# Performance work log

Measured on AMD Instinct MI355X. Metric: run time of the kernel, lower is better.

Reference implementation:

```python
import jax, jax.numpy as jnp
import numpy as np

N, H, C, E, R = 16384, 1024, 256, 16, 128
EPS = 1e-8


def setup_inputs() -> dict:
    key = jax.random.key(0)
    ks = jax.random.split(key, 8)
    s = 1.0 / np.sqrt(H)
    return {
        "x": jax.random.normal(ks[0], (N, H), jnp.float32),
        "Wd": jax.random.normal(ks[1], (H, C), jnp.float32) * s,
        "bd": jax.random.normal(ks[2], (C,), jnp.float32) * 0.01,
        "centroids": jax.random.uniform(ks[3], (E, C), jnp.float32),  # torch.rand
        "Wg": jax.random.normal(ks[4], (E, H, H), jnp.float32) * s,
        "bg": jax.random.normal(ks[5], (E, H), jnp.float32) * 0.01,
        "U": jax.random.normal(ks[6], (E, H, R), jnp.float32) * s,
        "V": jax.random.normal(ks[7], (E, R, H), jnp.float32) * (1.0 / np.sqrt(R)),
        "k": 2,
    }


def reference(x, Wd, bd, centroids, Wg, bg, U, V, k):
    # ---- Router ----
    distilled = jax.nn.gelu(x @ Wd + bd, approximate=False)          # [N, C]
    dn = distilled / jnp.maximum(
        jnp.linalg.norm(distilled, axis=-1, keepdims=True), EPS)
    cn = centroids / jnp.maximum(
        jnp.linalg.norm(centroids, axis=-1, keepdims=True), EPS)
    # cdist (euclidean) between dn [N,C] and cn [E,C]
    d2 = (jnp.sum(dn * dn, -1, keepdims=True)
          + jnp.sum(cn * cn, -1)[None, :]
          - 2.0 * (dn @ cn.T))                                        # [N, E]
    distances = jnp.sqrt(jnp.maximum(d2, 0.0))
    probabilities = jax.nn.softmax(-distances, axis=-1)               # [N, E]
    top_p, top_i = jax.lax.top_k(probabilities, k)                    # [N, k]
    # sparse combine weights: zero except at top-k experts
    combine = jnp.zeros((x.shape[0], E), x.dtype)
    combine = combine.at[jnp.arange(x.shape[0])[:, None], top_i].set(top_p)
    # ---- Expert dispatch: scan over experts (low-rank Highway blocks) ----
    def body(acc, params):
        Wg_e, bg_e, U_e, V_e, w_e = params
        gate = jax.nn.sigmoid(x @ Wg_e + bg_e)                        # [N, H]
        trans = (x @ U_e) @ V_e                                       # [N, H]
        y = gate * trans + (1.0 - gate) * x
        return acc + w_e[:, None] * y, None
    out, _ = jax.lax.scan(body, jnp.zeros_like(x),
                          (Wg, bg, U, V, combine.T))
    return out
```

## Files before the change

kernel.cpp:

```cpp
#include <hip/hip_runtime.h>
#include <hip/hip_bf16.h>
#include <hip/hip_fp16.h>
#include <cstdint>
#include <cstddef>

#define NTOK 16384
#define HD   1024
#define CD   256
#define NE   16
#define RD   128
#define MAXBLK 528
#define EGRID  2304

typedef __attribute__((ext_vector_type(8))) short bf16x8;
typedef __attribute__((ext_vector_type(4))) float f32x4;
typedef unsigned short u16;
typedef unsigned int u32;

__device__ __forceinline__ u16 f2bf(float f) {
    u32 u = __float_as_uint(f);
    u32 r = (u + 0x7FFFu + ((u >> 16) & 1u)) >> 16;
    return (u16)r;
}

__device__ __forceinline__ void gload16(const void* g, void* lds) {
    __builtin_amdgcn_global_load_lds((const __attribute__((address_space(1))) void*)g,
                                     (__attribute__((address_space(3))) void*)lds,
                                     16, 0, 0);
}

__device__ __forceinline__ float wredsum(float v) {
#pragma unroll
    for (int m = 32; m >= 1; m >>= 1) v += __shfl_xor(v, m, 64);
    return v;
}

__global__ __launch_bounds__(64) void centroid_norm_kernel(
    const float* __restrict__ cen, float* __restrict__ cn, float* __restrict__ sncn)
{
    int e = blockIdx.x, l = threadIdx.x;
    float4 c = *(const float4*)&cen[e * CD + l * 4];
    float ss = wredsum(c.x * c.x + c.y * c.y + c.z * c.z + c.w * c.w);
    float den = fmaxf(sqrtf(ss), 1e-8f);
    float4 n;
    n.x = c.x / den; n.y = c.y / den; n.z = c.z / den; n.w = c.w / den;
    *(float4*)&cn[e * CD + l * 4] = n;
    float s2 = wredsum(n.x * n.x + n.y * n.y + n.z * n.z + n.w * n.w);
    if (l == 0) sncn[e] = s2;
}

__global__ __launch_bounds__(256, 4) void router_gemm_kernel(
    const float* __restrict__ x, const float* __restrict__ Wd,
    const float* __restrict__ bd, float* __restrict__ dT)
{
    __shared__ float lA[16][128];
    __shared__ float lB[16][64];
    int tid = threadIdx.x;
    int rb = (blockIdx.x >> 2) * 128;
    int cb = (blockIdx.x & 3) * 64;
    int tx = tid & 15, ty = tid >> 4;
    int arow = tid >> 1, akq = (tid & 1) * 8;
    int bk = tid >> 4, bc = (tid & 15) * 4;
    float acc[8][4];
#pragma unroll
    for (int i = 0; i < 8; ++i)
#pragma unroll
        for (int j = 0; j < 4; ++j) acc[i][j] = 0.f;

    for (int k0 = 0; k0 < HD; k0 += 16) {
        float4 a0 = *(const float4*)&x[(size_t)(rb + arow) * HD + k0 + akq];
        float4 a1 = *(const float4*)&x[(size_t)(rb + arow) * HD + k0 + akq + 4];
        float4 bv = *(const float4*)&Wd[(size_t)(k0 + bk) * CD + cb + bc];
        __syncthreads();
        lA[akq + 0][arow] = a0.x; lA[akq + 1][arow] = a0.y;
        lA[akq + 2][arow] = a0.z; lA[akq + 3][arow] = a0.w;
        lA[akq + 4][arow] = a1.x; lA[akq + 5][arow] = a1.y;
        lA[akq + 6][arow] = a1.z; lA[akq + 7][arow] = a1.w;
        *(float4*)&lB[bk][bc] = bv;
        __syncthreads();
#pragma unroll
        for (int kk = 0; kk < 16; ++kk) {
            float4 va0 = *(const float4*)&lA[kk][ty * 8];
            float4 va1 = *(const float4*)&lA[kk][ty * 8 + 4];
            float4 vb  = *(const float4*)&lB[kk][tx * 4];
            float ar[8] = {va0.x, va0.y, va0.z, va0.w, va1.x, va1.y, va1.z, va1.w};
            float br[4] = {vb.x, vb.y, vb.z, vb.w};
#pragma unroll
            for (int i = 0; i < 8; ++i)
#pragma unroll
                for (int j = 0; j < 4; ++j) acc[i][j] = fmaf(ar[i], br[j], acc[i][j]);
        }
    }
#pragma unroll
    for (int j = 0; j < 4; ++j) {
        int c = cb + tx * 4 + j;
        float b = bd[c];
        float g[8];
#pragma unroll
        for (int i = 0; i < 8; ++i) {
            float v = acc[i][j] + b;
            g[i] = 0.5f * v * (1.f + erff(v * 0.70710678118654752f));
        }
        float4 w0 = {g[0], g[1], g[2], g[3]};
        float4 w1 = {g[4], g[5], g[6], g[7]};
        *(float4*)&dT[(size_t)c * NTOK + rb + ty * 8] = w0;
        *(float4*)&dT[(size_t)c * NTOK + rb + ty * 8 + 4] = w1;
    }
}

__global__ __launch_bounds__(256) void router_score_kernel(
    const float* __restrict__ dT, const float* __restrict__ cn,
    const float* __restrict__ sncn, int* __restrict__ top_i,
    float* __restrict__ top_w, int* __restrict__ counts)
{
    __shared__ float lcn[NE][CD];
    __shared__ float sdot[NE][64];
    __shared__ float sss[64];
    __shared__ int hist[NE];
    int tid = threadIdx.x, lane = tid & 63, w = tid >> 6;
    for (int i = tid; i < NE * CD / 4; i += 256)
        ((float4*)&lcn[0][0])[i] = ((const float4*)cn)[i];
    if (tid < NE) hist[tid] = 0;
    __syncthreads();

    int tokbase = blockIdx.x * 64;
    const float* p = dT + tokbase + lane;
    int e0 = w * 4;
    float d0 = 0.f, d1 = 0.f, d2a = 0.f, d3 = 0.f, ss = 0.f;
#pragma unroll 4
    for (int k = 0; k < CD; ++k) {
        float v = p[(size_t)k * NTOK];
        ss = fmaf(v, v, ss);
        d0 = fmaf(v, lcn[e0 + 0][k], d0);
        d1 = fmaf(v, lcn[e0 + 1][k], d1);
        d2a = fmaf(v, lcn[e0 + 2][k], d2a);
        d3 = fmaf(v, lcn[e0 + 3][k], d3);
    }
    sdot[e0 + 0][lane] = d0;
    sdot[e0 + 1][lane] = d1;
    sdot[e0 + 2][lane] = d2a;
    sdot[e0 + 3][lane] = d3;
    if (w == 0) sss[lane] = ss;
    __syncthreads();

    if (tid < 64) {
        int tok = tokbase + tid;
        float ssv = sss[tid];
        float den = fmaxf(sqrtf(ssv), 1e-8f);
        float inv = 1.f / den;
        float sndn = (ssv * inv) * inv;
        float pr[NE];
#pragma unroll
        for (int e = 0; e < NE; ++e) {
            float dotn = sdot[e][tid] * inv;
            float dd2 = sndn + sncn[e] - 2.f * dotn;
            pr[e] = -sqrtf(fmaxf(dd2, 0.f));
        }
        float mx = pr[0];
#pragma unroll
        for (int e = 1; e < NE; ++e) mx = fmaxf(mx, pr[e]);
        float sum = 0.f;
#pragma unroll
        for (int e = 0; e < NE; ++e) { pr[e] = expf(pr[e] - mx); sum += pr[e]; }
        float invs = 1.f / sum;
#pragma unroll
        for (int e = 0; e < NE; ++e) pr[e] *= invs;
        int i1 = 0; float p1 = pr[0];
#pragma unroll
        for (int e = 1; e < NE; ++e) if (pr[e] > p1) { p1 = pr[e]; i1 = e; }
        int i2 = -1; float p2 = -1.f;
#pragma unroll
        for (int e = 0; e < NE; ++e) if (e != i1 && pr[e] > p2) { p2 = pr[e]; i2 = e; }
        top_i[tok * 2 + 0] = i1; top_w[tok * 2 + 0] = p1;
        top_i[tok * 2 + 1] = i2; top_w[tok * 2 + 1] = p2;
        atomicAdd(&hist[i1], 1);
        atomicAdd(&hist[i2], 1);
    }
    __syncthreads();
    if (tid < NE) atomicAdd(&counts[tid], hist[tid]);
}

__global__ void scan_kernel(const int* __restrict__ counts, int* __restrict__ offsets,
                            int* __restrict__ blkstart, int* __restrict__ cursor)
{
    if (threadIdx.x == 0 && blockIdx.x == 0) {
        int o = 0, b = 0;
        for (int e = 0; e < NE; ++e) {
            offsets[e] = o; blkstart[e] = b; cursor[e] = 0;
            o += counts[e]; b += (counts[e] + 63) >> 6;
        }
        offsets[NE] = o; blkstart[NE] = b;
    }
}

__global__ __launch_bounds__(256) void build_lists_kernel(
    const int* __restrict__ top_i, const float* __restrict__ top_w,
    const int* __restrict__ offsets, int* __restrict__ cursor,
    int* __restrict__ list_tok, float* __restrict__ list_w)
{
    int t = blockIdx.x * 256 + threadIdx.x;
#pragma unroll
    for (int j = 0; j < 2; ++j) {
        int e = top_i[t * 2 + j];
        int pos = atomicAdd(&cursor[e], 1);
        int idx = offsets[e] + pos;
        list_tok[idx] = t;
        list_w[idx] = top_w[t * 2 + j];
    }
}

__global__ __launch_bounds__(256) void cvt_bf16_kernel(
    const float* __restrict__ src, u16* __restrict__ dst, int n4)
{
    int i = blockIdx.x * 256 + threadIdx.x;
    if (i >= n4) return;
    float4 v = *(const float4*)&src[(size_t)i * 4];
    ushort4 o;
    o.x = f2bf(v.x); o.y = f2bf(v.y); o.z = f2bf(v.z); o.w = f2bf(v.w);
    *(ushort4*)&dst[(size_t)i * 4] = o;
}

__global__ __launch_bounds__(256) void transpose_cvt_kernel(
    const float* __restrict__ src, u16* __restrict__ dst, int K, int N)
{
    __shared__ float t[32][33];
    const float* s = src + (size_t)blockIdx.z * K * N;
    u16* d = dst + (size_t)blockIdx.z * K * N;
    int kb = blockIdx.y * 32, nb = blockIdx.x * 32;
    int r = threadIdx.x >> 3, c4 = (threadIdx.x & 7) * 4;
    float4 v = *(const float4*)&s[(size_t)(kb + r) * N + nb + c4];
    t[r][c4 + 0] = v.x; t[r][c4 + 1] = v.y; t[r][c4 + 2] = v.z; t[r][c4 + 3] = v.w;
    __syncthreads();
    ushort4 o;
    o.x = f2bf(t[c4 + 0][r]); o.y = f2bf(t[c4 + 1][r]);
    o.z = f2bf(t[c4 + 2][r]); o.w = f2bf(t[c4 + 3][r]);
    *(ushort4*)&d[(size_t)(nb + r) * K + kb + c4] = o;
}


__global__ __launch_bounds__(256, 3) void tproj_kernel(
    const u16* __restrict__ xbf, const u16* __restrict__ uT,
    const int* __restrict__ list_tok, const int* __restrict__ offsets,
    const int* __restrict__ blkstart, u16* __restrict__ tbf)
{
    __shared__ __align__(16) u16 lds[2 * 6144];
    __shared__ int s_tok[64];
    int mb = blockIdx.x;
    int e = 0;
#pragma unroll
    for (int i = 0; i < NE; ++i) if (mb >= blkstart[i + 1]) e = i + 1;
    if (e >= NE) return;
    int mloc = (mb - blkstart[e]) * 64;
    int base = offsets[e] + mloc;
    int cnt = offsets[e + 1] - offsets[e];
    int mv = min(64, cnt - mloc);
    int tid = threadIdx.x, lane = tid & 63, w = tid >> 6;
    if (tid < 64) s_tok[tid] = list_tok[base + (tid < mv ? tid : 0)];
    __syncthreads();
    int lrow = lane >> 2;
    int sl = (lane & 3) ^ ((lane >> 3) & 3);
    int rr = lane & 15, hi = lane >> 4;
    int rslot = hi ^ ((rr >> 1) & 3);
    const u16* uE = uT + (size_t)e * RD * HD;

    const u16* gb[3]; char* lp[3];
#pragma unroll
    for (int i = 0; i < 3; ++i) {
        int idx = w + 4 * i;
        if (idx < 4) {
            gb[i] = xbf + (size_t)s_tok[idx * 16 + lrow] * HD + sl * 8;
            lp[i] = (char*)lds + idx * 1024;
        } else {
            int bi = idx - 4;
            gb[i] = uE + (size_t)(bi * 16 + lrow) * HD + sl * 8;
            lp[i] = (char*)lds + 4096 + bi * 1024;
        }
    }
    const f32x4 zz = {0.f, 0.f, 0.f, 0.f};
    f32x4 acc[4][2];
#pragma unroll
    for (int im = 0; im < 4; ++im)
#pragma unroll
        for (int in = 0; in < 2; ++in) acc[im][in] = zz;

    auto STAGE = [&](int buf, int t) {
#pragma unroll
        for (int i = 0; i < 3; ++i) gload16(gb[i] + t * 32, lp[i] + buf * 12288);
    };
    auto COMP = [&](int buf, f32x4 (&a)[4][2]) {
        const u16* LA = lds + buf * 6144;
        const u16* LB = LA + 2048;
        bf16x8 af[4], bfv[2];
#pragma unroll
        for (int im = 0; im < 4; ++im) af[im] = *(const bf16x8*)&LA[(im * 16 + rr) * 32 + rslot * 8];
#pragma unroll
        for (int in = 0; in < 2; ++in) bfv[in] = *(const bf16x8*)&LB[(w * 32 + in * 16 + rr) * 32 + rslot * 8];
#pragma unroll
        for (int im = 0; im < 4; ++im)
#pragma unroll
            for (int in = 0; in < 2; ++in)
                a[im][in] = __builtin_amdgcn_mfma_f32_16x16x32_bf16(af[im], bfv[in], a[im][in], 0, 0, 0);
    };

    STAGE(0, 0);
    __syncthreads();
    for (int t = 0; t < 31; ++t) {
        STAGE((t + 1) & 1, t + 1);
        COMP(t & 1, acc);
        __syncthreads();
    }
    COMP(1, acc);

#pragma unroll
    for (int im = 0; im < 4; ++im)
#pragma unroll
        for (int in = 0; in < 2; ++in)
#pragma unroll
            for (int j = 0; j < 4; ++j) {
                int r = im * 16 + hi * 4 + j;
                if (r < mv) {
                    int c = w * 32 + in * 16 + rr;
                    tbf[(size_t)(base + r) * RD + c] = f2bf(acc[im][in][j]);
                }
            }
}

__global__ __launch_bounds__(256, 3) void expert_kernel(
    const u16* __restrict__ xbf, const u16* __restrict__ wgT,
    const u16* __restrict__ vT, const u16* __restrict__ tbf,
    const float* __restrict__ x, const float* __restrict__ bg,
    const int* __restrict__ list_tok, const float* __restrict__ list_w,
    const int* __restrict__ offsets, const int* __restrict__ blkstart,
    float* __restrict__ out)
{
    __shared__ __align__(16) u16 lds[2 * 10240];
    __shared__ int s_tok[64];
    __shared__ float s_w[64];
    int d = blockIdx.x;
    int l = (d >> 8) * 256 + (d & 7) * 32 + ((d & 255) >> 3);
    if (l >= 4 * MAXBLK) return;
    int ct = l / MAXBLK;
    int mb = l % MAXBLK;
    int e = 0;
#pragma unroll
    for (int i = 0; i < NE; ++i) if (mb >= blkstart[i + 1]) e = i + 1;
    if (e >= NE) return;
    int mloc = (mb - blkstart[e]) * 64;
    int base = offsets[e] + mloc;
    int cnt = offsets[e + 1] - offsets[e];
    int mv = min(64, cnt - mloc);
    int tid = threadIdx.x, lane = tid & 63, w = tid >> 6;
    if (tid < 64) {
        int p = base + (tid < mv ? tid : 0);
        s_tok[tid] = list_tok[p];
        s_w[tid] = (tid < mv) ? list_w[p] : 0.f;
    }
    __syncthreads();
    int lrow = lane >> 2;
    int sl = (lane & 3) ^ ((lane >> 3) & 3);
    int rr = lane & 15, hi = lane >> 4;
    int rslot = hi ^ ((rr >> 1) & 3);

    const u16* wgE = wgT + (size_t)e * HD * HD + (size_t)(ct * 256) * HD;
    const u16* vE  = vT  + (size_t)e * HD * RD + (size_t)(ct * 256) * RD;

    char* lp[5];
    const u16* gbT[5]; const u16* gbG[5];
#pragma unroll
    for (int i = 0; i < 5; ++i) {
        int idx = w + 4 * i;
        if (idx < 4) {
            lp[i]  = (char*)lds + idx * 1024;
            gbT[i] = tbf + (size_t)(base + idx * 16 + lrow) * RD + sl * 8;
            gbG[i] = xbf + (size_t)s_tok[idx * 16 + lrow] * HD + sl * 8;
        } else {
            int bi = idx - 4;
            lp[i]  = (char*)lds + 4096 + bi * 1024;
            gbT[i] = vE  + (size_t)(bi * 16 + lrow) * RD + sl * 8;
            gbG[i] = wgE + (size_t)(bi * 16 + lrow) * HD + sl * 8;
        }
    }

    auto STAGE = [&](int buf, int t, const u16* const (&gb)[5]) {
#pragma unroll
        for (int i = 0; i < 5; ++i) gload16(gb[i] + t * 32, lp[i] + buf * 20480);
    };
    auto COMP = [&](int buf, f32x4 (&a)[4][4]) {
        const u16* LA = lds + buf * 10240;
        const u16* LB = LA + 2048;
        bf16x8 af[4], bfv[4];
#pragma unroll
        for (int im = 0; im < 4; ++im) af[im] = *(const bf16x8*)&LA[(im * 16 + rr) * 32 + rslot * 8];
#pragma unroll
        for (int in = 0; in < 4; ++in) bfv[in] = *(const bf16x8*)&LB[(w * 64 + in * 16 + rr) * 32 + rslot * 8];
#pragma unroll
        for (int im = 0; im < 4; ++im)
#pragma unroll
            for (int in = 0; in < 4; ++in)
                a[im][in] = __builtin_amdgcn_mfma_f32_16x16x32_bf16(af[im], bfv[in], a[im][in], 0, 0, 0);
    };

    const f32x4 zz = {0.f, 0.f, 0.f, 0.f};
    float bgv[4];
#pragma unroll
    for (int in = 0; in < 4; ++in)
        bgv[in] = bg[e * HD + ct * 256 + w * 64 + in * 16 + rr];

    f32x4 accG[4][4];
#pragma unroll
    for (int im = 0; im < 4; ++im)
#pragma unroll
        for (int in = 0; in < 4; ++in) accG[im][in] = zz;

    STAGE(0, 0, gbG);
    __syncthreads();
    for (int t = 0; t < 32; ++t) {
        if (t < 31) STAGE((t + 1) & 1, t + 1, gbG);
        else        STAGE(0, 0, gbT);
        COMP(t & 1, accG);
        __syncthreads();
    }

    __half2 sgp[4][4][2];
#pragma unroll
    for (int im = 0; im < 4; ++im)
#pragma unroll
        for (int in = 0; in < 4; ++in) {
            float s0 = 1.f / (1.f + __expf(-(accG[im][in][0] + bgv[in])));
            float s1 = 1.f / (1.f + __expf(-(accG[im][in][1] + bgv[in])));
            float s2 = 1.f / (1.f + __expf(-(accG[im][in][2] + bgv[in])));
            float s3 = 1.f / (1.f + __expf(-(accG[im][in][3] + bgv[in])));
            sgp[im][in][0] = __floats2half2_rn(s0, s1);
            sgp[im][in][1] = __floats2half2_rn(s2, s3);
        }

    f32x4 accT[4][4];
#pragma unroll
    for (int im = 0; im < 4; ++im)
#pragma unroll
        for (int in = 0; in < 4; ++in) accT[im][in] = zz;

#pragma unroll
    for (int s = 0; s < 4; ++s) {
        if (s < 3) STAGE((s + 1) & 1, s + 1, gbT);
        COMP(s & 1, accT);
        __syncthreads();
    }

#pragma unroll
    for (int im = 0; im < 4; ++im)
#pragma unroll
        for (int j = 0; j < 4; ++j) {
            int r = im * 16 + hi * 4 + j;
            if (r < mv) {
                int tok = s_tok[r];
                float wgt = s_w[r];
                size_t rowoff = (size_t)tok * HD;
#pragma unroll
                for (int in = 0; in < 4; ++in) {
                    int c = ct * 256 + w * 64 + in * 16 + rr;
                    float2 sq = __half22float2(sgp[im][in][j >> 1]);
                    float sg = (j & 1) ? sq.y : sq.x;
                    float tr = accT[im][in][j];
                    float xv = x[rowoff + c];
                    float yv = sg * tr + (1.f - sg) * xv;
                    atomicAdd(&out[rowoff + c], wgt * yv);
                }
            }
        }
}

extern "C" void kernel_launch(void* const* d_in, const int* in_sizes, int n_in,
                              void* d_out, int out_size, void* d_ws, size_t ws_size,
                              hipStream_t stream)
{
    const float* x   = (const float*)d_in[0];
    const float* Wd  = (const float*)d_in[1];
    const float* bd  = (const float*)d_in[2];
    const float* cen = (const float*)d_in[3];
    const float* Wg  = (const float*)d_in[4];
    const float* bg  = (const float*)d_in[5];
    const float* U   = (const float*)d_in[6];
    const float* V   = (const float*)d_in[7];
    float* out = (float*)d_out;

    char* ws = (char*)d_ws;
    size_t off = 0;
    auto alloc = [&](size_t bytes) { size_t o = off; off = (off + bytes + 255) & ~(size_t)255; return o; };
    float* dT        = (float*)(ws + alloc((size_t)NTOK * CD * 4));
    float* cn        = (float*)(ws + alloc((size_t)NE * CD * 4));
    float* sncn      = (float*)(ws + alloc(NE * 4));
    int*   top_i     = (int*)(ws + alloc((size_t)NTOK * 2 * 4));
    float* top_w     = (float*)(ws + alloc((size_t)NTOK * 2 * 4));
    int*   counts    = (int*)(ws + alloc(NE * 4));
    int*   offsets   = (int*)(ws + alloc((NE + 1) * 4));
    int*   blkstart  = (int*)(ws + alloc((NE + 1) * 4));
    int*   cursor    = (int*)(ws + alloc(NE * 4));
    int*   list_tok  = (int*)(ws + alloc((size_t)NTOK * 2 * 4));
    float* list_w    = (float*)(ws + alloc((size_t)NTOK * 2 * 4));
    u16*   xbf       = (u16*)(ws + alloc((size_t)NTOK * HD * 2));
    u16*   wgT       = (u16*)(ws + alloc((size_t)NE * HD * HD * 2));
    u16*   uT        = (u16*)(ws + alloc((size_t)NE * RD * HD * 2));
    u16*   vT        = (u16*)(ws + alloc((size_t)NE * RD * HD * 2));
    u16*   tbf       = (u16*)(ws + alloc(((size_t)NTOK * 2 + 64) * RD * 2));

    hipMemsetAsync(out, 0, (size_t)out_size * 4, stream);
    hipMemsetAsync(counts, 0, NE * 4, stream);

    centroid_norm_kernel<<<NE, 64, 0, stream>>>(cen, cn, sncn);
    router_gemm_kernel<<<(NTOK / 128) * 4, 256, 0, stream>>>(x, Wd, bd, dT);
    router_score_kernel<<<NTOK / 64, 256, 0, stream>>>(dT, cn, sncn, top_i, top_w, counts);
    scan_kernel<<<1, 64, 0, stream>>>(counts, offsets, blkstart, cursor);
    build_lists_kernel<<<NTOK / 256, 256, 0, stream>>>(top_i, top_w, offsets, cursor, list_tok, list_w);

    cvt_bf16_kernel<<<(NTOK * HD / 4 + 255) / 256, 256, 0, stream>>>(x, xbf, NTOK * HD / 4);
    transpose_cvt_kernel<<<dim3(HD / 32, HD / 32, NE), 256, 0, stream>>>(Wg, wgT, HD, HD);
    transpose_cvt_kernel<<<dim3(RD / 32, HD / 32, NE), 256, 0, stream>>>(U, uT, HD, RD);
    transpose_cvt_kernel<<<dim3(HD / 32, RD / 32, NE), 256, 0, stream>>>(V, vT, RD, HD);

    tproj_kernel<<<MAXBLK, 256, 0, stream>>>(xbf, uT, list_tok, offsets, blkstart, tbf);
    expert_kernel<<<EGRID, 256, 0, stream>>>(xbf, wgT, vT, tbf, x, bg,
                                             list_tok, list_w, offsets, blkstart, out);
}
```

Measured before the change: 601.8 us.

## Retile expert GEMMs to 128x128 blocks and compute low-rank path first

Changes the token-block size from 64 to 128 rows and the column tile from 256 to 128, using a 2x2 warp layout in both tproj and expert kernels. The blocks are more square, so each loaded weight tile and token tile is reused across more outputs. In the expert kernel, the low-rank transform GEMM now runs first and is kept as packed fp16, and the sigmoid is computed in the epilogue from the gate accumulators. The trade-offs are more padding waste in experts whose token counts are not multiples of 128, and a higher register load from holding both accumulator sets.

```diff
diff --git a/kernel.cpp b/kernel.cpp
--- a/kernel.cpp
+++ b/kernel.cpp
@@ -9,7 +9,8 @@
 #define CD   256
 #define NE   16
 #define RD   128
-#define MAXBLK 528
+#define MB2    272
+#define LOGB   2176
 #define EGRID  2304
 
 typedef __attribute__((ext_vector_type(8))) short bf16x8;
@@ -187,7 +188,7 @@
         int o = 0, b = 0;
         for (int e = 0; e < NE; ++e) {
             offsets[e] = o; blkstart[e] = b; cursor[e] = 0;
-            o += counts[e]; b += (counts[e] + 63) >> 6;
+            o += counts[e]; b += (counts[e] + 127) >> 7;
         }
         offsets[NE] = o; blkstart[NE] = b;
     }
@@ -243,62 +244,64 @@
     const int* __restrict__ list_tok, const int* __restrict__ offsets,
     const int* __restrict__ blkstart, u16* __restrict__ tbf)
 {
-    __shared__ __align__(16) u16 lds[2 * 6144];
-    __shared__ int s_tok[64];
+    __shared__ __align__(16) u16 lds[2 * 8192];
+    __shared__ int s_tok[128];
     int mb = blockIdx.x;
     int e = 0;
 #pragma unroll
     for (int i = 0; i < NE; ++i) if (mb >= blkstart[i + 1]) e = i + 1;
     if (e >= NE) return;
-    int mloc = (mb - blkstart[e]) * 64;
+    int mloc = (mb - blkstart[e]) * 128;
     int base = offsets[e] + mloc;
     int cnt = offsets[e + 1] - offsets[e];
-    int mv = min(64, cnt - mloc);
+    int mv = min(128, cnt - mloc);
     int tid = threadIdx.x, lane = tid & 63, w = tid >> 6;
-    if (tid < 64) s_tok[tid] = list_tok[base + (tid < mv ? tid : 0)];
+    if (tid < 128) s_tok[tid] = list_tok[base + (tid < mv ? tid : 0)];
     __syncthreads();
     int lrow = lane >> 2;
     int sl = (lane & 3) ^ ((lane >> 3) & 3);
     int rr = lane & 15, hi = lane >> 4;
     int rslot = hi ^ ((rr >> 1) & 3);
+    int wr = w >> 1, wc = w & 1;
     const u16* uE = uT + (size_t)e * RD * HD;
 
-    const u16* gb[3]; char* lp[3];
-#pragma unroll
-    for (int i = 0; i < 3; ++i) {
+    const u16* gb[4]; char* lp[4];
+#pragma unroll
+    for (int i = 0; i < 4; ++i) {
         int idx = w + 4 * i;
-        if (idx < 4) {
-            gb[i] = xbf + (size_t)s_tok[idx * 16 + lrow] * HD + sl * 8;
+        if (idx < 8) {
+            int row = idx * 16 + lrow;
+            gb[i] = xbf + (size_t)s_tok[row] * HD + sl * 8;
             lp[i] = (char*)lds + idx * 1024;
         } else {
-            int bi = idx - 4;
-            gb[i] = uE + (size_t)(bi * 16 + lrow) * HD + sl * 8;
-            lp[i] = (char*)lds + 4096 + bi * 1024;
+            int row = (idx - 8) * 16 + lrow;
+            gb[i] = uE + (size_t)row * HD + sl * 8;
+            lp[i] = (char*)lds + 8192 + (idx - 8) * 1024;
         }
     }
     const f32x4 zz = {0.f, 0.f, 0.f, 0.f};
-    f32x4 acc[4][2];
+    f32x4 acc[4][4];
 #pragma unroll
     for (int im = 0; im < 4; ++im)
 #pragma unroll
-        for (int in = 0; in < 2; ++in) acc[im][in] = zz;
+        for (int in = 0; in < 4; ++in) acc[im][in] = zz;
 
     auto STAGE = [&](int buf, int t) {
 #pragma unroll
-        for (int i = 0; i < 3; ++i) gload16(gb[i] + t * 32, lp[i] + buf * 12288);
+        for (int i = 0; i < 4; ++i) gload16(gb[i] + t * 32, lp[i] + buf * 16384);
     };
-    auto COMP = [&](int buf, f32x4 (&a)[4][2]) {
-        const u16* LA = lds + buf * 6144;
-        const u16* LB = LA + 2048;
-        bf16x8 af[4], bfv[2];
-#pragma unroll
-        for (int im = 0; im < 4; ++im) af[im] = *(const bf16x8*)&LA[(im * 16 + rr) * 32 + rslot * 8];
-#pragma unroll
-        for (int in = 0; in < 2; ++in) bfv[in] = *(const bf16x8*)&LB[(w * 32 + in * 16 + rr) * 32 + rslot * 8];
+    auto COMP = [&](int buf, f32x4 (&a)[4][4]) {
+        const u16* LA = lds + buf * 8192;
+        const u16* LB = LA + 4096;
+        bf16x8 af[4], bfv[4];
+#pragma unroll
+        for (int im = 0; im < 4; ++im) af[im] = *(const bf16x8*)&LA[(wr * 64 + im * 16 + rr) * 32 + rslot * 8];
+#pragma unroll
+        for (int in = 0; in < 4; ++in) bfv[in] = *(const bf16x8*)&LB[(wc * 64 + in * 16 + rr) * 32 + rslot * 8];
 #pragma unroll
         for (int im = 0; im < 4; ++im)
 #pragma unroll
-            for (int in = 0; in < 2; ++in)
+            for (int in = 0; in < 4; ++in)
                 a[im][in] = __builtin_amdgcn_mfma_f32_16x16x32_bf16(af[im], bfv[in], a[im][in], 0, 0, 0);
     };
 
@@ -314,12 +317,12 @@
 #pragma unroll
     for (int im = 0; im < 4; ++im)
 #pragma unroll
-        for (int in = 0; in < 2; ++in)
+        for (int in = 0; in < 4; ++in)
 #pragma unroll
             for (int j = 0; j < 4; ++j) {
-                int r = im * 16 + hi * 4 + j;
+                int r = wr * 64 + im * 16 + hi * 4 + j;
                 if (r < mv) {
-                    int c = w * 32 + in * 16 + rr;
+                    int c = wc * 64 + in * 16 + rr;
                     tbf[(size_t)(base + r) * RD + c] = f2bf(acc[im][in][j]);
                 }
             }
@@ -333,24 +336,23 @@
     const int* __restrict__ offsets, const int* __restrict__ blkstart,
     float* __restrict__ out)
 {
-    __shared__ __align__(16) u16 lds[2 * 10240];
-    __shared__ int s_tok[64];
-    __shared__ float s_w[64];
+    __shared__ __align__(16) u16 lds[2 * 8192];
+    __shared__ int s_tok[128];
+    __shared__ float s_w[128];
     int d = blockIdx.x;
     int l = (d >> 8) * 256 + (d & 7) * 32 + ((d & 255) >> 3);
-    if (l >= 4 * MAXBLK) return;
-    int ct = l / MAXBLK;
-    int mb = l % MAXBLK;
+    if (l >= LOGB) return;
+    int mb = l >> 3, ct = l & 7;
     int e = 0;
 #pragma unroll
     for (int i = 0; i < NE; ++i) if (mb >= blkstart[i + 1]) e = i + 1;
     if (e >= NE) return;
-    int mloc = (mb - blkstart[e]) * 64;
+    int mloc = (mb - blkstart[e]) * 128;
     int base = offsets[e] + mloc;
     int cnt = offsets[e + 1] - offsets[e];
-    int mv = min(64, cnt - mloc);
+    int mv = min(128, cnt - mloc);
     int tid = threadIdx.x, lane = tid & 63, w = tid >> 6;
-    if (tid < 64) {
+    if (tid < 128) {
         int p = base + (tid < mv ? tid : 0);
         s_tok[tid] = list_tok[p];
         s_w[tid] = (tid < mv) ? list_w[p] : 0.f;
@@ -360,39 +362,41 @@
     int sl = (lane & 3) ^ ((lane >> 3) & 3);
     int rr = lane & 15, hi = lane >> 4;
     int rslot = hi ^ ((rr >> 1) & 3);
-
-    const u16* wgE = wgT + (size_t)e * HD * HD + (size_t)(ct * 256) * HD;
-    const u16* vE  = vT  + (size_t)e * HD * RD + (size_t)(ct * 256) * RD;
-
-    char* lp[5];
-    const u16* gbT[5]; const u16* gbG[5];
-#pragma unroll
-    for (int i = 0; i < 5; ++i) {
+    int wr = w >> 1, wc = w & 1;
+
+    const u16* wgE = wgT + (size_t)e * HD * HD + (size_t)(ct * 128) * HD;
+    const u16* vE  = vT  + (size_t)e * HD * RD + (size_t)(ct * 128) * RD;
+
+    char* lp[4];
+    const u16* gbT[4]; const u16* gbG[4];
+#pragma unroll
+    for (int i = 0; i < 4; ++i) {
         int idx = w + 4 * i;
-        if (idx < 4) {
+        if (idx < 8) {
+            int row = idx * 16 + lrow;
             lp[i]  = (char*)lds + idx * 1024;
-            gbT[i] = tbf + (size_t)(base + idx * 16 + lrow) * RD + sl * 8;
-            gbG[i] = xbf + (size_t)s_tok[idx * 16 + lrow] * HD + sl * 8;
+            gbT[i] = tbf + (size_t)(base + (row < mv ? row : 0)) * RD + sl * 8;
+            gbG[i] = xbf + (size_t)s_tok[row] * HD + sl * 8;
         } else {
-            int bi = idx - 4;
-            lp[i]  = (char*)lds + 4096 + bi * 1024;
-            gbT[i] = vE  + (size_t)(bi * 16 + lrow) * RD + sl * 8;
-            gbG[i] = wgE + (size_t)(bi * 16 + lrow) * HD + sl * 8;
-        }
-    }
-
-    auto STAGE = [&](int buf, int t, const u16* const (&gb)[5]) {
-#pragma unroll
-        for (int i = 0; i < 5; ++i) gload16(gb[i] + t * 32, lp[i] + buf * 20480);
+            int row = (idx - 8) * 16 + lrow;
+            lp[i]  = (char*)lds + 8192 + (idx - 8) * 1024;
+            gbT[i] = vE  + (size_t)row * RD + sl * 8;
+            gbG[i] = wgE + (size_t)row * HD + sl * 8;
+        }
+    }
+
+    auto STAGE = [&](int buf, int t, const u16* const (&gb)[4]) {
+#pragma unroll
+        for (int i = 0; i < 4; ++i) gload16(gb[i] + t * 32, lp[i] + buf * 16384);
     };
     auto COMP = [&](int buf, f32x4 (&a)[4][4]) {
-        const u16* LA = lds + buf * 10240;
-        const u16* LB = LA + 2048;
+        const u16* LA = lds + buf * 8192;
+        const u16* LB = LA + 4096;
         bf16x8 af[4], bfv[4];
 #pragma unroll
-        for (int im = 0; im < 4; ++im) af[im] = *(const bf16x8*)&LA[(im * 16 + rr) * 32 + rslot * 8];
-#pragma unroll
-        for (int in = 0; in < 4; ++in) bfv[in] = *(const bf16x8*)&LB[(w * 64 + in * 16 + rr) * 32 + rslot * 8];
+        for (int im = 0; im < 4; ++im) af[im] = *(const bf16x8*)&LA[(wr * 64 + im * 16 + rr) * 32 + rslot * 8];
+#pragma unroll
+        for (int in = 0; in < 4; ++in) bfv[in] = *(const bf16x8*)&LB[(wc * 64 + in * 16 + rr) * 32 + rslot * 8];
 #pragma unroll
         for (int im = 0; im < 4; ++im)
 #pragma unroll
@@ -401,10 +405,30 @@
     };
 
     const f32x4 zz = {0.f, 0.f, 0.f, 0.f};
-    float bgv[4];
-#pragma unroll
-    for (int in = 0; in < 4; ++in)
-        bgv[in] = bg[e * HD + ct * 256 + w * 64 + in * 16 + rr];
+    f32x4 accT[4][4];
+#pragma unroll
+    for (int im = 0; im < 4; ++im)
+#pragma unroll
+        for (int in = 0; in < 4; ++in) accT[im][in] = zz;
+
+    STAGE(0, 0, gbT);
+    __syncthreads();
+#pragma unroll
+    for (int s = 0; s < 4; ++s) {
+        if (s < 3) STAGE((s + 1) & 1, s + 1, gbT);
+        else       STAGE(0, 0, gbG);
+        COMP(s & 1, accT);
+        __syncthreads();
+    }
+
+    __half2 tpk[4][4][2];
+#pragma unroll
+    for (int im = 0; im < 4; ++im)
+#pragma unroll
+        for (int in = 0; in < 4; ++in) {
+            tpk[im][in][0] = __floats2half2_rn(accT[im][in][0], accT[im][in][1]);
+            tpk[im][in][1] = __floats2half2_rn(accT[im][in][2], accT[im][in][3]);
+        }
 
     f32x4 accG[4][4];
 #pragma unroll
@@ -412,56 +436,34 @@
 #pragma unroll
         for (int in = 0; in < 4; ++in) accG[im][in] = zz;
 
-    STAGE(0, 0, gbG);
-    __syncthreads();
-    for (int t = 0; t < 32; ++t) {
-        if (t < 31) STAGE((t + 1) & 1, t + 1, gbG);
-        else        STAGE(0, 0, gbT);
+    for (int t = 0; t < 31; ++t) {
+        STAGE((t + 1) & 1, t + 1, gbG);
         COMP(t & 1, accG);
         __syncthreads();
     }
-
-    __half2 sgp[4][4][2];
+    COMP(1, accG);
+
+    float bgv[4];
+#pragma unroll
+    for (int in = 0; in < 4; ++in)
+        bgv[in] = bg[e * HD + ct * 128 + wc * 64 + in * 16 + rr];
+
 #pragma unroll
     for (int im = 0; im < 4; ++im)
 #pragma unroll
-        for (int in = 0; in < 4; ++in) {
-            float s0 = 1.f / (1.f + __expf(-(accG[im][in][0] + bgv[in])));
-            float s1 = 1.f / (1.f + __expf(-(accG[im][in][1] + bgv[in])));
-            float s2 = 1.f / (1.f + __expf(-(accG[im][in][2] + bgv[in])));
-            float s3 = 1.f / (1.f + __expf(-(accG[im][in][3] + bgv[in])));
-            sgp[im][in][0] = __floats2half2_rn(s0, s1);
-            sgp[im][in][1] = __floats2half2_rn(s2, s3);
-        }
-
-    f32x4 accT[4][4];
-#pragma unroll
-    for (int im = 0; im < 4; ++im)
-#pragma unroll
-        for (int in = 0; in < 4; ++in) accT[im][in] = zz;
-
-#pragma unroll
-    for (int s = 0; s < 4; ++s) {
-        if (s < 3) STAGE((s + 1) & 1, s + 1, gbT);
-        COMP(s & 1, accT);
-        __syncthreads();
-    }
-
-#pragma unroll
-    for (int im = 0; im < 4; ++im)
-#pragma unroll
         for (int j = 0; j < 4; ++j) {
-            int r = im * 16 + hi * 4 + j;
+            int r = wr * 64 + im * 16 + hi * 4 + j;
             if (r < mv) {
                 int tok = s_tok[r];
                 float wgt = s_w[r];
                 size_t rowoff = (size_t)tok * HD;
 #pragma unroll
                 for (int in = 0; in < 4; ++in) {
-                    int c = ct * 256 + w * 64 + in * 16 + rr;
-                    float2 sq = __half22float2(sgp[im][in][j >> 1]);
-                    float sg = (j & 1) ? sq.y : sq.x;
-                    float tr = accT[im][in][j];
+                    int c = ct * 128 + wc * 64 + in * 16 + rr;
+                    float gp = accG[im][in][j] + bgv[in];
+                    float sg = 1.f / (1.f + __expf(-gp));
+                    float2 tq = __half22float2(tpk[im][in][j >> 1]);
+                    float tr = (j & 1) ? tq.y : tq.x;
                     float xv = x[rowoff + c];
                     float yv = sg * tr + (1.f - sg) * xv;
                     atomicAdd(&out[rowoff + c], wgt * yv);
@@ -502,7 +504,7 @@
     u16*   wgT       = (u16*)(ws + alloc((size_t)NE * HD * HD * 2));
     u16*   uT        = (u16*)(ws + alloc((size_t)NE * RD * HD * 2));
     u16*   vT        = (u16*)(ws + alloc((size_t)NE * RD * HD * 2));
-    u16*   tbf       = (u16*)(ws + alloc(((size_t)NTOK * 2 + 64) * RD * 2));
+    u16*   tbf       = (u16*)(ws + alloc(((size_t)NTOK * 2 + 128) * RD * 2));
 
     hipMemsetAsync(out, 0, (size_t)out_size * 4, stream);
     hipMemsetAsync(counts, 0, NE * 4, stream);
@@ -518,7 +520,7 @@
     transpose_cvt_kernel<<<dim3(RD / 32, HD / 32, NE), 256, 0, stream>>>(U, uT, HD, RD);
     transpose_cvt_kernel<<<dim3(HD / 32, RD / 32, NE), 256, 0, stream>>>(V, vT, RD, HD);
 
-    tproj_kernel<<<MAXBLK, 256, 0, stream>>>(xbf, uT, list_tok, offsets, blkstart, tbf);
+    tproj_kernel<<<MB2, 256, 0, stream>>>(xbf, uT, list_tok, offsets, blkstart, tbf);
     expert_kernel<<<EGRID, 256, 0, stream>>>(xbf, wgT, vT, tbf, x, bg,
                                              list_tok, list_w, offsets, blkstart, out);
 }
```

Result: faster. 563.4 us (-6.4%).
